# Kernel optimization log

Hardware: AMD Instinct MI355X
Metric: run time of the kernel (lower is better)

## Reference

```python
import jax, jax.numpy as jnp
import numpy as np

LN_EPS = 1e-5


def setup_inputs() -> dict:
    key = jax.random.key(0)
    k1, = jax.random.split(key, 1)
    B, C, H, W = 16, 512, 64, 64
    HW = H * W
    x = jax.random.normal(k1, (B, C, H, W), dtype=jnp.float32)
    gamma = jnp.ones((), dtype=jnp.float32)          # Scale(1) learnable scalar
    ln_weight = jnp.ones((HW,), dtype=jnp.float32)   # LayerNorm weight
    ln_bias = jnp.zeros((HW,), dtype=jnp.float32)    # LayerNorm bias
    return {"x": x, "gamma": gamma, "ln_weight": ln_weight, "ln_bias": ln_bias}


def reference(x, gamma, ln_weight, ln_bias):
    B, C, H, W = x.shape
    v = x.reshape(B, C, H * W)                       # [B, C, HW] (Q = K = V)
    energy = jnp.einsum('bcn,bdn->bcd', v, v)        # [B, C, C]
    attn = jax.nn.softmax(energy, axis=-1)
    out = jnp.einsum('bcd,bdn->bcn', attn, v)        # [B, C, HW]
    out = gamma * out + v                            # scale + residual
    # LayerNorm over last dim (HW), torch eps=1e-5
    mean = jnp.mean(out, axis=-1, keepdims=True)
    var = jnp.mean(jnp.square(out - mean), axis=-1, keepdims=True)
    out = (out - mean) * jax.lax.rsqrt(var + LN_EPS) * ln_weight + ln_bias
    return out.reshape(B, C, H, W)
```

## Files before the change

### kernel.cpp

```cpp
#include <hip/hip_runtime.h>
#include <hip/hip_bf16.h>

#define B_DIM 16
#define C_DIM 512
#define HW_DIM 4096
#define LN_EPS 1e-5f
#define ATTN_STRIDE 1024

using bf16 = __hip_bfloat16;
typedef __bf16 v8bf __attribute__((ext_vector_type(8)));
typedef float v4f __attribute__((ext_vector_type(4)));
typedef unsigned short v8us __attribute__((ext_vector_type(8)));
typedef unsigned short v4us __attribute__((ext_vector_type(4)));
using gptr_t = const __attribute__((address_space(1))) void*;
using lptr_t = __attribute__((address_space(3))) void*;

__device__ __forceinline__ unsigned short f2bf(float f) {
  unsigned int u = __float_as_uint(f);
  u = (u + 0x7fffu + ((u >> 16) & 1u)) >> 16;
  return (unsigned short)u;
}
__device__ __forceinline__ float bf2f(unsigned short us) {
  return __uint_as_float(((unsigned int)us) << 16);
}

__global__ __launch_bounds__(256) void k_convert(
    const float* __restrict__ x, unsigned short* __restrict__ v) {
  const size_t i0 = ((size_t)blockIdx.x * 256 + threadIdx.x) * 8;
  const size_t step = (size_t)2048 * 256 * 8;
#pragma unroll
  for (int it = 0; it < 8; ++it) {
    const size_t base = i0 + (size_t)it * step;
    const float4 f0 = ((const float4*)(x + base))[0];
    const float4 f1 = ((const float4*)(x + base))[1];
    v8us pack;
    pack[0] = f2bf(f0.x); pack[1] = f2bf(f0.y);
    pack[2] = f2bf(f0.z); pack[3] = f2bf(f0.w);
    pack[4] = f2bf(f1.x); pack[5] = f2bf(f1.y);
    pack[6] = f2bf(f1.z); pack[7] = f2bf(f1.w);
    *(v8us*)(v + base) = pack;
  }
}

#define TILE_E (256 * 64)

__device__ __forceinline__ void stage_half8(
    const bf16* __restrict__ g, bf16* l, int k0, int stride, int wave, int lane) {
  const int lrow = lane >> 3, lc = lane & 7;
#pragma unroll
  for (int i = 0; i < 2; ++i) {
    const int row = i * 64 + wave * 8 + lrow;
    __builtin_amdgcn_global_load_lds(
        (gptr_t)(g + (size_t)row * stride + k0 + ((lc ^ (row & 7)) << 3)),
        (lptr_t)(l + (i * 64 + wave * 8) * 64), 16, 0, 0);
  }
}
__device__ __forceinline__ void stage_op2(
    const bf16* __restrict__ g, bf16* l, int k0, int stride, int wave, int lane) {
  stage_half8(g, l, k0, stride, wave, lane);
  stage_half8(g + (size_t)128 * stride, l + 128 * 64, k0, stride, wave, lane);
}
__device__ __forceinline__ v8bf ld_frag8(const bf16* l, int row, int j) {
  return *(const v8bf*)(l + row * 64 + ((j ^ (row & 7)) << 3));
}
__device__ __forceinline__ v8bf ld_frag8B(const bf16* l, int row, int j) {
  const int key = (row & 7) ^ ((row >> 3) & 7);
  return *(const v8bf*)(l + row * 64 + ((j ^ key) << 3));
}
__device__ __forceinline__ void stageA8(
    const bf16* __restrict__ g, bf16* l, int k0, int stride,
    int w4, int lrow, int lc) {
#pragma unroll
  for (int i = 0; i < 8; ++i) {
    const int row = i * 32 + w4 * 8 + lrow;
    __builtin_amdgcn_global_load_lds(
        (gptr_t)(g + (size_t)row * stride + k0 + ((lc ^ (row & 7)) << 3)),
        (lptr_t)(l + (i * 32 + w4 * 8) * 64), 16, 0, 0);
  }
}
__device__ __forceinline__ void bwrite8(
    bf16* lb, const v8us bu[8], int dblk, int n8) {
  unsigned short* lu = (unsigned short*)lb;
#pragma unroll
  for (int j = 0; j < 8; ++j) {
    const int n = n8 + j;
    const int key = (n & 7) ^ ((n >> 3) & 7);
    v8us p;
#pragma unroll
    for (int r = 0; r < 8; ++r) p[r] = bu[r][j];
    *(v8us*)(lu + n * 64 + ((dblk ^ key) << 3)) = p;
  }
}

__device__ __forceinline__ void gemm_8ph_loop(
    const bf16* __restrict__ Ab, const bf16* __restrict__ Bb,
    const int strideA, const int strideB, const int kts,
    bf16* smem, const int wave, const int lane, v4f acc[8][4]) {
  const int wm = wave >> 2, wn = wave & 3;
  const int rl = lane & 15, kq = lane >> 4;

  stage_op2(Bb, smem + 2 * TILE_E, 0, strideB, wave, lane);
  stage_op2(Ab, smem, 0, strideA, wave, lane);
  stage_op2(Bb, smem + 3 * TILE_E, 64, strideB, wave, lane);
  stage_op2(Ab, smem + TILE_E, 64, strideA, wave, lane);
  asm volatile("s_waitcnt vmcnt(8)" ::: "memory");
  __builtin_amdgcn_s_barrier();

  v8bf a[4][2], b01[2][2], b23[2][2];
  for (int kt = 0; kt < kts; ++kt) {
    const bf16* LA = smem + (kt & 1) * TILE_E;
    const bf16* LB = smem + (2 + (kt & 1)) * TILE_E;
    bf16* SA = smem + (kt & 1) * TILE_E;
    bf16* SB = smem + (2 + (kt & 1)) * TILE_E;
#pragma unroll
    for (int mi = 0; mi < 4; ++mi)
#pragma unroll
      for (int kk = 0; kk < 2; ++kk)
        a[mi][kk] = ld_frag8(LA, wm * 128 + mi * 16 + rl, kk * 4 + kq);
#pragma unroll
    for (int ni = 0; ni < 2; ++ni)
#pragma unroll
      for (int kk = 0; kk < 2; ++kk)
        b01[ni][kk] = ld_frag8(LB, wn * 64 + ni * 16 + rl, kk * 4 + kq);
    __builtin_amdgcn_s_barrier();
    asm volatile("s_waitcnt lgkmcnt(0)");
    __builtin_amdgcn_s_setprio(1);
#pragma unroll
    for (int kk = 0; kk < 2; ++kk)
#pragma unroll
      for (int mi = 0; mi < 4; ++mi)
#pragma unroll
        for (int ni = 0; ni < 2; ++ni)
          acc[mi][ni] = __builtin_amdgcn_mfma_f32_16x16x32_bf16(
              a[mi][kk], b01[ni][kk], acc[mi][ni], 0, 0, 0);
    __builtin_amdgcn_s_setprio(0);
    __builtin_amdgcn_s_barrier();
#pragma unroll
    for (int ni = 0; ni < 2; ++ni)
#pragma unroll
      for (int kk = 0; kk < 2; ++kk)
        b23[ni][kk] = ld_frag8(LB, wn * 64 + (ni + 2) * 16 + rl, kk * 4 + kq);
    __builtin_amdgcn_s_barrier();
    asm volatile("s_waitcnt lgkmcnt(0)");
    __builtin_amdgcn_s_setprio(1);
#pragma unroll
    for (int kk = 0; kk < 2; ++kk)
#pragma unroll
      for (int mi = 0; mi < 4; ++mi)
#pragma unroll
        for (int ni = 0; ni < 2; ++ni)
          acc[mi][ni + 2] = __builtin_amdgcn_mfma_f32_16x16x32_bf16(
              a[mi][kk], b23[ni][kk], acc[mi][ni + 2], 0, 0, 0);
    __builtin_amdgcn_s_setprio(0);
    __builtin_amdgcn_s_barrier();
#pragma unroll
    for (int mi = 0; mi < 4; ++mi)
#pragma unroll
      for (int kk = 0; kk < 2; ++kk)
        a[mi][kk] = ld_frag8(LA, wm * 128 + (mi + 4) * 16 + rl, kk * 4 + kq);
    if (kt < kts - 2) stage_op2(Bb, SB, (kt + 2) * 64, strideB, wave, lane);
    __builtin_amdgcn_s_barrier();
    asm volatile("s_waitcnt lgkmcnt(0)");
    __builtin_amdgcn_s_setprio(1);
#pragma unroll
    for (int kk = 0; kk < 2; ++kk)
#pragma unroll
      for (int mi = 0; mi < 4; ++mi)
#pragma unroll
        for (int ni = 0; ni < 2; ++ni)
          acc[mi + 4][ni + 2] = __builtin_amdgcn_mfma_f32_16x16x32_bf16(
              a[mi][kk], b23[ni][kk], acc[mi + 4][ni + 2], 0, 0, 0);
    __builtin_amdgcn_s_setprio(0);
    __builtin_amdgcn_s_barrier();
    if (kt < kts - 2) stage_op2(Ab, SA, (kt + 2) * 64, strideA, wave, lane);
    __builtin_amdgcn_s_barrier();
    __builtin_amdgcn_s_setprio(1);
#pragma unroll
    for (int kk = 0; kk < 2; ++kk)
#pragma unroll
      for (int mi = 0; mi < 4; ++mi)
#pragma unroll
        for (int ni = 0; ni < 2; ++ni)
          acc[mi + 4][ni] = __builtin_amdgcn_mfma_f32_16x16x32_bf16(
              a[mi][kk], b01[ni][kk], acc[mi + 4][ni], 0, 0, 0);
    __builtin_amdgcn_s_setprio(0);
    if (kt < kts - 2)
      asm volatile("s_waitcnt vmcnt(8)" ::: "memory");
    else if (kt == kts - 2)
      asm volatile("s_waitcnt vmcnt(0)" ::: "memory");
    __builtin_amdgcn_s_barrier();
  }
}

__device__ __forceinline__ void epilogue_bounce(
    v4f acc[8][4], bf16* smem, float* ob, const int out_stride,
    const int wave, const int lane) {
  const int wm = wave >> 2, wn = wave & 3;
  const int rl = lane & 15, kq = lane >> 4;
  float* smf = (float*)smem;
#pragma unroll
  for (int h = 0; h < 2; ++h) {
    if (wm == h) {
#pragma unroll
      for (int mi = 0; mi < 8; ++mi)
#pragma unroll
        for (int ni = 0; ni < 4; ++ni)
#pragma unroll
          for (int rr = 0; rr < 4; ++rr) {
            const int rloc = mi * 16 + kq * 4 + rr;
            const int col = wn * 64 + ni * 16 + rl;
            const int key = rloc & 7;
            smf[rloc * 256 + ((((col >> 2) ^ key) << 2) | (col & 3))] =
                acc[mi][ni][rr];
          }
    }
    __syncthreads();
#pragma unroll
    for (int it = 0; it < 16; ++it) {
      const int rloc = it * 8 + wave;
      const float4 vv =
          *(const float4*)(smf + rloc * 256 + ((lane ^ (rloc & 7)) << 2));
      *(float4*)(ob + (size_t)(h * 128 + rloc) * out_stride + lane * 4) = vv;
    }
    __syncthreads();
  }
}

__global__ __launch_bounds__(512, 2) void k_gemm1(
    const bf16* __restrict__ v, float* __restrict__ e_part) {
  __shared__ __align__(16) bf16 smem[4 * TILE_E];
  const int bid = blockIdx.x;
  const int t = (bid & 7) * 32 + (bid >> 3);
  const int ks = t & 3;
  const int db = (t >> 2) & 1;
  const int cb = (t >> 3) & 1;
  const int b = t >> 4;
  const int tid = threadIdx.x;
  const int wave = tid >> 6, lane = tid & 63;

  const bf16* vb = v + (size_t)b * ((size_t)C_DIM * HW_DIM) + ks * 1024;
  const bf16* Ab = vb + (size_t)(cb * 256) * HW_DIM;
  const bf16* Bb = vb + (size_t)(db * 256) * HW_DIM;

  v4f acc[8][4] = {};
  gemm_8ph_loop(Ab, Bb, HW_DIM, HW_DIM, 16, smem, wave, lane, acc);

  float* ob = e_part + (size_t)ks * ((size_t)B_DIM * C_DIM * C_DIM) +
              (size_t)b * (C_DIM * C_DIM) + (size_t)(cb * 256) * C_DIM + db * 256;
  epilogue_bounce(acc, smem, ob, C_DIM, wave, lane);
}

__global__ __launch_bounds__(256) void k_softmax(
    const float* __restrict__ e_part, unsigned short* __restrict__ attn) {
  const int row = blockIdx.x;
  const size_t bcc = (size_t)B_DIM * C_DIM * C_DIM;
  const float* e0 = e_part + (size_t)row * C_DIM;
  const int tid = threadIdx.x;
  float v0 = 0.f, v1 = 0.f;
#pragma unroll
  for (int p = 0; p < 4; ++p) {
    v0 += e0[p * bcc + tid];
    v1 += e0[p * bcc + tid + 256];
  }
  float mx = fmaxf(v0, v1);
#pragma unroll
  for (int off = 32; off > 0; off >>= 1) mx = fmaxf(mx, __shfl_xor(mx, off));
  __shared__ float rmax[4], rsum[4];
  const int wv = tid >> 6, ln = tid & 63;
  if (ln == 0) rmax[wv] = mx;
  __syncthreads();
  mx = fmaxf(fmaxf(rmax[0], rmax[1]), fmaxf(rmax[2], rmax[3]));
  const float p0 = __expf(v0 - mx), p1 = __expf(v1 - mx);
  float s = p0 + p1;
#pragma unroll
  for (int off = 32; off > 0; off >>= 1) s += __shfl_xor(s, off);
  if (ln == 0) rsum[wv] = s;
  __syncthreads();
  s = rsum[0] + rsum[1] + rsum[2] + rsum[3];
  const float inv = 1.0f / s;
  attn[(size_t)row * ATTN_STRIDE + tid] = f2bf(p0 * inv);
  attn[(size_t)row * ATTN_STRIDE + tid + 256] = f2bf(p1 * inv);
}

__global__ __launch_bounds__(512, 2) void k_gemm2(
    const bf16* __restrict__ attn, const bf16* __restrict__ v,
    float* __restrict__ out) {
  __shared__ __align__(16) bf16 smem[4 * TILE_E];
  const int bid = blockIdx.x;
  const int t = (bid & 7) * 64 + (bid >> 3);
  const int b = t >> 5;
  const int cb = (t >> 4) & 1;
  const int nb = t & 15;
  const int tid = threadIdx.x;
  const int wave = tid >> 6, lane = tid & 63;
  const int rl = lane & 15, kq = lane >> 4;
  const int wm = wave >> 2, wn = wave & 3;

  const bf16* Ab = attn + (size_t)(b * C_DIM + cb * 256) * ATTN_STRIDE;
  const bf16* Vb = v + (size_t)b * ((size_t)C_DIM * HW_DIM) + nb * 256;

  const bool isB = (tid < 256);
  const int w4 = wave & 3;
  const int lrow = lane >> 3, lc = lane & 7;
  const int dblk = (tid & 255) >> 5;
  const int n8 = (tid & 31) * 8;

  v4f acc[8][4] = {};
  v8us bu[8];

  if (isB) {
#pragma unroll
    for (int r = 0; r < 8; ++r)
      bu[r] = *(const v8us*)((const unsigned short*)Vb +
                             (size_t)(dblk * 8 + r) * HW_DIM + n8);
    bwrite8(smem + 2 * TILE_E, bu, dblk, n8);
#pragma unroll
    for (int r = 0; r < 8; ++r)
      bu[r] = *(const v8us*)((const unsigned short*)Vb +
                             (size_t)(64 + dblk * 8 + r) * HW_DIM + n8);
    bwrite8(smem + 3 * TILE_E, bu, dblk, n8);
  } else {
    stageA8(Ab, smem, 0, ATTN_STRIDE, w4, lrow, lc);
    stageA8(Ab, smem + TILE_E, 64, ATTN_STRIDE, w4, lrow, lc);
  }
  asm volatile("s_waitcnt vmcnt(8)" ::: "memory");
  __builtin_amdgcn_s_barrier();

  v8bf a[4][2], b01[2][2], b23[2][2];
  for (int kt = 0; kt < 8; ++kt) {
    const bf16* LA = smem + (kt & 1) * TILE_E;
    const bf16* LB = smem + (2 + (kt & 1)) * TILE_E;
    bf16* SA = smem + (kt & 1) * TILE_E;
    bf16* SB = smem + (2 + (kt & 1)) * TILE_E;
#pragma unroll
    for (int mi = 0; mi < 4; ++mi)
#pragma unroll
      for (int kk = 0; kk < 2; ++kk)
        a[mi][kk] = ld_frag8(LA, wm * 128 + mi * 16 + rl, kk * 4 + kq);
#pragma unroll
    for (int ni = 0; ni < 2; ++ni)
#pragma unroll
      for (int kk = 0; kk < 2; ++kk)
        b01[ni][kk] = ld_frag8B(LB, wn * 64 + ni * 16 + rl, kk * 4 + kq);
    if (isB && kt < 6) {
      const int d0 = (kt + 2) * 64 + dblk * 8;
#pragma unroll
      for (int r = 0; r < 8; ++r)
        bu[r] = *(const v8us*)((const unsigned short*)Vb +
                               (size_t)(d0 + r) * HW_DIM + n8);
    }
    __builtin_amdgcn_s_barrier();
    asm volatile("s_waitcnt lgkmcnt(0)");
    __builtin_amdgcn_s_setprio(1);
#pragma unroll
    for (int kk = 0; kk < 2; ++kk)
#pragma unroll
      for (int mi = 0; mi < 4; ++mi)
#pragma unroll
        for (int ni = 0; ni < 2; ++ni)
          acc[mi][ni] = __builtin_amdgcn_mfma_f32_16x16x32_bf16(
              a[mi][kk], b01[ni][kk], acc[mi][ni], 0, 0, 0);
    __builtin_amdgcn_s_setprio(0);
    __builtin_amdgcn_s_barrier();
#pragma unroll
    for (int ni = 0; ni < 2; ++ni)
#pragma unroll
      for (int kk = 0; kk < 2; ++kk)
        b23[ni][kk] = ld_frag8B(LB, wn * 64 + (ni + 2) * 16 + rl, kk * 4 + kq);
    __builtin_amdgcn_s_barrier();
    asm volatile("s_waitcnt lgkmcnt(0)");
    __builtin_amdgcn_s_setprio(1);
#pragma unroll
    for (int kk = 0; kk < 2; ++kk)
#pragma unroll
      for (int mi = 0; mi < 4; ++mi)
#pragma unroll
        for (int ni = 0; ni < 2; ++ni)
          acc[mi][ni + 2] = __builtin_amdgcn_mfma_f32_16x16x32_bf16(
              a[mi][kk], b23[ni][kk], acc[mi][ni + 2], 0, 0, 0);
    __builtin_amdgcn_s_setprio(0);
    __builtin_amdgcn_s_barrier();
#pragma unroll
    for (int mi = 0; mi < 4; ++mi)
#pragma unroll
      for (int kk = 0; kk < 2; ++kk)
        a[mi][kk] = ld_frag8(LA, wm * 128 + (mi + 4) * 16 + rl, kk * 4 + kq);
    if (isB && kt < 6) bwrite8(SB, bu, dblk, n8);
    __builtin_amdgcn_s_barrier();
    asm volatile("s_waitcnt lgkmcnt(0)");
    __builtin_amdgcn_s_setprio(1);
#pragma unroll
    for (int kk = 0; kk < 2; ++kk)
#pragma unroll
      for (int mi = 0; mi < 4; ++mi)
#pragma unroll
        for (int ni = 0; ni < 2; ++ni)
          acc[mi + 4][ni + 2] = __builtin_amdgcn_mfma_f32_16x16x32_bf16(
              a[mi][kk], b23[ni][kk], acc[mi + 4][ni + 2], 0, 0, 0);
    __builtin_amdgcn_s_setprio(0);
    __builtin_amdgcn_s_barrier();
    if (!isB && kt < 6)
      stageA8(Ab, SA, (kt + 2) * 64, ATTN_STRIDE, w4, lrow, lc);
    __builtin_amdgcn_s_barrier();
    __builtin_amdgcn_s_setprio(1);
#pragma unroll
    for (int kk = 0; kk < 2; ++kk)
#pragma unroll
      for (int mi = 0; mi < 4; ++mi)
#pragma unroll
        for (int ni = 0; ni < 2; ++ni)
          acc[mi + 4][ni] = __builtin_amdgcn_mfma_f32_16x16x32_bf16(
              a[mi][kk], b01[ni][kk], acc[mi + 4][ni], 0, 0, 0);
    __builtin_amdgcn_s_setprio(0);
    if (kt < 6)
      asm volatile("s_waitcnt vmcnt(8)" ::: "memory");
    else if (kt == 6)
      asm volatile("s_waitcnt vmcnt(0)" ::: "memory");
    __builtin_amdgcn_s_barrier();
  }

  float* ob = out + (size_t)b * ((size_t)C_DIM * HW_DIM) +
              (size_t)(cb * 256) * HW_DIM + nb * 256;
  epilogue_bounce(acc, smem, ob, HW_DIM, wave, lane);
}

__global__ __launch_bounds__(256) void k_ln(
    float* __restrict__ out, const unsigned short* __restrict__ vres,
    const float* __restrict__ gamma, const float* __restrict__ w,
    const float* __restrict__ bias) {
  const int row = blockIdx.x;
  float* p = out + (size_t)row * HW_DIM;
  const unsigned short* vr = vres + (size_t)row * HW_DIM;
  const float g = gamma[0];
  const int tid = threadIdx.x;
  float4 vals[4];
  float s = 0.f, ss = 0.f;
#pragma unroll
  for (int i = 0; i < 4; ++i) {
    const int idx = tid + i * 256;
    const float4 av = ((const float4*)p)[idx];
    const v4us rv = *(const v4us*)(vr + idx * 4);
    float4 vv;
    vv.x = g * av.x + bf2f(rv[0]);
    vv.y = g * av.y + bf2f(rv[1]);
    vv.z = g * av.z + bf2f(rv[2]);
    vv.w = g * av.w + bf2f(rv[3]);
    vals[i] = vv;
    s += vv.x + vv.y + vv.z + vv.w;
    ss += vv.x * vv.x + vv.y * vv.y + vv.z * vv.z + vv.w * vv.w;
  }
#pragma unroll
  for (int off = 32; off > 0; off >>= 1) {
    s += __shfl_xor(s, off);
    ss += __shfl_xor(ss, off);
  }
  __shared__ float rs[4], rss[4];
  const int wv = tid >> 6, ln = tid & 63;
  if (ln == 0) { rs[wv] = s; rss[wv] = ss; }
  __syncthreads();
  s = rs[0] + rs[1] + rs[2] + rs[3];
  ss = rss[0] + rss[1] + rss[2] + rss[3];
  const float mean = s * (1.f / HW_DIM);
  const float var = ss * (1.f / HW_DIM) - mean * mean;
  const float rstd = rsqrtf(var + LN_EPS);
#pragma unroll
  for (int i = 0; i < 4; ++i) {
    const int idx = tid + i * 256;
    const float4 vv = vals[i];
    const float4 w4 = ((const float4*)w)[idx];
    const float4 b4 = ((const float4*)bias)[idx];
    float4 r;
    r.x = (vv.x - mean) * rstd * w4.x + b4.x;
    r.y = (vv.y - mean) * rstd * w4.y + b4.y;
    r.z = (vv.z - mean) * rstd * w4.z + b4.z;
    r.w = (vv.w - mean) * rstd * w4.w + b4.w;
    ((float4*)p)[idx] = r;
  }
}

extern "C" void kernel_launch(void* const* d_in, const int* in_sizes, int n_in,
                              void* d_out, int out_size, void* d_ws, size_t ws_size,
                              hipStream_t stream) {
  const float* x = (const float*)d_in[0];
  const float* gamma = (const float*)d_in[1];
  const float* lnw = (const float*)d_in[2];
  const float* lnb = (const float*)d_in[3];
  float* out = (float*)d_out;
  char* ws = (char*)d_ws;

  const size_t n_elem = (size_t)B_DIM * C_DIM * HW_DIM;
  unsigned short* vbf = (unsigned short*)ws;
  float* e_part = (float*)(ws + 4 * n_elem);
  unsigned short* attn = (unsigned short*)e_part;

  k_convert<<<2048, 256, 0, stream>>>(x, vbf);
  k_gemm1<<<256, 512, 0, stream>>>((const bf16*)vbf, e_part);
  k_softmax<<<B_DIM * C_DIM, 256, 0, stream>>>(e_part, attn);
  k_gemm2<<<512, 512, 0, stream>>>((const bf16*)attn, (const bf16*)vbf, out);
  k_ln<<<B_DIM * C_DIM, 256, 0, stream>>>(out, vbf, gamma, lnw, lnb);
}
```

Measured before the change: 243.4 us.

## Pre-transpose V during conversion, use async LDS loads in gemm2, emit bf16 intermediate

The conversion kernel now also writes a transposed bf16 copy of V ([n, c] layout) through a swizzled shared-memory tile. gemm2 can then stage both operands with global_load_lds, which replaces the register-based transpose and bwrite8 path. Attention rows are packed at stride C instead of 1024. gemm2 writes its output as bf16 into a workspace buffer rather than fp32 to the output, which halves that write and the matching read in the LayerNorm kernel. In exchange it adds an extra 64 MB transposed write and lowers the precision of the attention output before the residual and LayerNorm.

```diff
diff --git a/kernel.cpp b/kernel.cpp
--- a/kernel.cpp
+++ b/kernel.cpp
@@ -5,7 +5,6 @@
 #define C_DIM 512
 #define HW_DIM 4096
 #define LN_EPS 1e-5f
-#define ATTN_STRIDE 1024
 
 using bf16 = __hip_bfloat16;
 typedef __bf16 v8bf __attribute__((ext_vector_type(8)));
@@ -24,27 +23,58 @@
   return __uint_as_float(((unsigned int)us) << 16);
 }
 
-__global__ __launch_bounds__(256) void k_convert(
-    const float* __restrict__ x, unsigned short* __restrict__ v) {
-  const size_t i0 = ((size_t)blockIdx.x * 256 + threadIdx.x) * 8;
-  const size_t step = (size_t)2048 * 256 * 8;
-#pragma unroll
-  for (int it = 0; it < 8; ++it) {
-    const size_t base = i0 + (size_t)it * step;
-    const float4 f0 = ((const float4*)(x + base))[0];
-    const float4 f1 = ((const float4*)(x + base))[1];
+__global__ __launch_bounds__(256) void k_convert_transpose(
+    const float* __restrict__ x, unsigned short* __restrict__ v,
+    unsigned short* __restrict__ vt) {
+  __shared__ unsigned short tile[64 * 64];
+  const int tid = threadIdx.x;
+  const int b = blockIdx.z;
+  const int n0 = blockIdx.x * 64;
+  const int c0 = blockIdx.y * 64;
+  const size_t boff = (size_t)b * ((size_t)C_DIM * HW_DIM);
+  const float* xb = x + boff;
+  unsigned short* vb = v + boff;
+  unsigned short* vtb = vt + boff;
+
+  const int cl = tid >> 3;
+  const int hb = tid & 7;
+  const int h8 = hb * 8;
+#pragma unroll
+  for (int j = 0; j < 2; ++j) {
+    const int c = cl + j * 32;
+    const float* src = xb + (size_t)(c0 + c) * HW_DIM + n0 + h8;
+    const float4 f0 = ((const float4*)src)[0];
+    const float4 f1 = ((const float4*)src)[1];
     v8us pack;
     pack[0] = f2bf(f0.x); pack[1] = f2bf(f0.y);
     pack[2] = f2bf(f0.z); pack[3] = f2bf(f0.w);
     pack[4] = f2bf(f1.x); pack[5] = f2bf(f1.y);
     pack[6] = f2bf(f1.z); pack[7] = f2bf(f1.w);
-    *(v8us*)(v + base) = pack;
-  }
+    *(v8us*)(vb + (size_t)(c0 + c) * HW_DIM + n0 + h8) = pack;
+    const int key = (c & 7) ^ ((c >> 3) & 7);
+    *(v8us*)(tile + c * 64 + ((hb ^ key) << 3)) = pack;
+  }
+  __syncthreads();
+  const int nl = tid >> 3;
+  const int c8 = (tid & 7) * 8;
+  const int n = 2 * nl;
+  v8us pa, pb;
+#pragma unroll
+  for (int e = 0; e < 8; ++e) {
+    const int r = c8 + e;
+    const int key = (r & 7) ^ ((r >> 3) & 7);
+    const unsigned int w = *(const unsigned int*)(
+        tile + r * 64 + (((n >> 3) ^ key) << 3) + (n & 7));
+    pa[e] = (unsigned short)(w & 0xffffu);
+    pb[e] = (unsigned short)(w >> 16);
+  }
+  *(v8us*)(vtb + (size_t)(n0 + n) * C_DIM + c0 + c8) = pa;
+  *(v8us*)(vtb + (size_t)(n0 + n + 1) * C_DIM + c0 + c8) = pb;
 }
 
 #define TILE_E (256 * 64)
 
-__device__ __forceinline__ void stage_half8(
+__device__ __forceinline__ void stage_half8s(
     const bf16* __restrict__ g, bf16* l, int k0, int stride, int wave, int lane) {
   const int lrow = lane >> 3, lc = lane & 7;
 #pragma unroll
@@ -55,41 +85,29 @@
         (lptr_t)(l + (i * 64 + wave * 8) * 64), 16, 0, 0);
   }
 }
+__device__ __forceinline__ void stage_op2s(
+    const bf16* __restrict__ g, bf16* l, int k0, int stride, int wave, int lane) {
+  stage_half8s(g, l, k0, stride, wave, lane);
+  stage_half8s(g + (size_t)128 * stride, l + 128 * 64, k0, stride, wave, lane);
+}
+__device__ __forceinline__ void stage_half8(
+    const bf16* __restrict__ g, bf16* l, int k0, int wave, int lane) {
+  const int lrow = lane >> 3, lc = lane & 7;
+#pragma unroll
+  for (int i = 0; i < 2; ++i) {
+    const int row = i * 64 + wave * 8 + lrow;
+    __builtin_amdgcn_global_load_lds(
+        (gptr_t)(g + (size_t)row * C_DIM + k0 + ((lc ^ (row & 7)) << 3)),
+        (lptr_t)(l + (i * 64 + wave * 8) * 64), 16, 0, 0);
+  }
+}
 __device__ __forceinline__ void stage_op2(
-    const bf16* __restrict__ g, bf16* l, int k0, int stride, int wave, int lane) {
-  stage_half8(g, l, k0, stride, wave, lane);
-  stage_half8(g + (size_t)128 * stride, l + 128 * 64, k0, stride, wave, lane);
+    const bf16* __restrict__ g, bf16* l, int k0, int wave, int lane) {
+  stage_half8(g, l, k0, wave, lane);
+  stage_half8(g + (size_t)128 * C_DIM, l + 128 * 64, k0, wave, lane);
 }
 __device__ __forceinline__ v8bf ld_frag8(const bf16* l, int row, int j) {
   return *(const v8bf*)(l + row * 64 + ((j ^ (row & 7)) << 3));
-}
-__device__ __forceinline__ v8bf ld_frag8B(const bf16* l, int row, int j) {
-  const int key = (row & 7) ^ ((row >> 3) & 7);
-  return *(const v8bf*)(l + row * 64 + ((j ^ key) << 3));
-}
-__device__ __forceinline__ void stageA8(
-    const bf16* __restrict__ g, bf16* l, int k0, int stride,
-    int w4, int lrow, int lc) {
-#pragma unroll
-  for (int i = 0; i < 8; ++i) {
-    const int row = i * 32 + w4 * 8 + lrow;
-    __builtin_amdgcn_global_load_lds(
-        (gptr_t)(g + (size_t)row * stride + k0 + ((lc ^ (row & 7)) << 3)),
-        (lptr_t)(l + (i * 32 + w4 * 8) * 64), 16, 0, 0);
-  }
-}
-__device__ __forceinline__ void bwrite8(
-    bf16* lb, const v8us bu[8], int dblk, int n8) {
-  unsigned short* lu = (unsigned short*)lb;
-#pragma unroll
-  for (int j = 0; j < 8; ++j) {
-    const int n = n8 + j;
-    const int key = (n & 7) ^ ((n >> 3) & 7);
-    v8us p;
-#pragma unroll
-    for (int r = 0; r < 8; ++r) p[r] = bu[r][j];
-    *(v8us*)(lu + n * 64 + ((dblk ^ key) << 3)) = p;
-  }
 }
 
 __device__ __forceinline__ void gemm_8ph_loop(
@@ -99,10 +117,10 @@
   const int wm = wave >> 2, wn = wave & 3;
   const int rl = lane & 15, kq = lane >> 4;
 
-  stage_op2(Bb, smem + 2 * TILE_E, 0, strideB, wave, lane);
-  stage_op2(Ab, smem, 0, strideA, wave, lane);
-  stage_op2(Bb, smem + 3 * TILE_E, 64, strideB, wave, lane);
-  stage_op2(Ab, smem + TILE_E, 64, strideA, wave, lane);
+  stage_op2s(Bb, smem + 2 * TILE_E, 0, strideB, wave, lane);
+  stage_op2s(Ab, smem, 0, strideA, wave, lane);
+  stage_op2s(Bb, smem + 3 * TILE_E, 64, strideB, wave, lane);
+  stage_op2s(Ab, smem + TILE_E, 64, strideA, wave, lane);
   asm volatile("s_waitcnt vmcnt(8)" ::: "memory");
   __builtin_amdgcn_s_barrier();
 
@@ -158,7 +176,7 @@
 #pragma unroll
       for (int kk = 0; kk < 2; ++kk)
         a[mi][kk] = ld_frag8(LA, wm * 128 + (mi + 4) * 16 + rl, kk * 4 + kq);
-    if (kt < kts - 2) stage_op2(Bb, SB, (kt + 2) * 64, strideB, wave, lane);
+    if (kt < kts - 2) stage_op2s(Bb, SB, (kt + 2) * 64, strideB, wave, lane);
     __builtin_amdgcn_s_barrier();
     asm volatile("s_waitcnt lgkmcnt(0)");
     __builtin_amdgcn_s_setprio(1);
@@ -172,7 +190,7 @@
               a[mi][kk], b23[ni][kk], acc[mi + 4][ni + 2], 0, 0, 0);
     __builtin_amdgcn_s_setprio(0);
     __builtin_amdgcn_s_barrier();
-    if (kt < kts - 2) stage_op2(Ab, SA, (kt + 2) * 64, strideA, wave, lane);
+    if (kt < kts - 2) stage_op2s(Ab, SA, (kt + 2) * 64, strideA, wave, lane);
     __builtin_amdgcn_s_barrier();
     __builtin_amdgcn_s_setprio(1);
 #pragma unroll
@@ -278,13 +296,13 @@
   __syncthreads();
   s = rsum[0] + rsum[1] + rsum[2] + rsum[3];
   const float inv = 1.0f / s;
-  attn[(size_t)row * ATTN_STRIDE + tid] = f2bf(p0 * inv);
-  attn[(size_t)row * ATTN_STRIDE + tid + 256] = f2bf(p1 * inv);
+  attn[(size_t)row * C_DIM + tid] = f2bf(p0 * inv);
+  attn[(size_t)row * C_DIM + tid + 256] = f2bf(p1 * inv);
 }
 
 __global__ __launch_bounds__(512, 2) void k_gemm2(
-    const bf16* __restrict__ attn, const bf16* __restrict__ v,
-    float* __restrict__ out) {
+    const bf16* __restrict__ attn, const bf16* __restrict__ vt,
+    unsigned short* __restrict__ av) {
   __shared__ __align__(16) bf16 smem[4 * TILE_E];
   const int bid = blockIdx.x;
   const int t = (bid & 7) * 64 + (bid >> 3);
@@ -293,36 +311,18 @@
   const int nb = t & 15;
   const int tid = threadIdx.x;
   const int wave = tid >> 6, lane = tid & 63;
+  const int wm = wave >> 2, wn = wave & 3;
   const int rl = lane & 15, kq = lane >> 4;
-  const int wm = wave >> 2, wn = wave & 3;
-
-  const bf16* Ab = attn + (size_t)(b * C_DIM + cb * 256) * ATTN_STRIDE;
-  const bf16* Vb = v + (size_t)b * ((size_t)C_DIM * HW_DIM) + nb * 256;
-
-  const bool isB = (tid < 256);
-  const int w4 = wave & 3;
-  const int lrow = lane >> 3, lc = lane & 7;
-  const int dblk = (tid & 255) >> 5;
-  const int n8 = (tid & 31) * 8;
+
+  const bf16* Ab = attn + (size_t)b * (C_DIM * C_DIM) + (size_t)(cb * 256) * C_DIM;
+  const bf16* Bb = vt + (size_t)b * ((size_t)C_DIM * HW_DIM) + (size_t)(nb * 256) * C_DIM;
 
   v4f acc[8][4] = {};
-  v8us bu[8];
-
-  if (isB) {
-#pragma unroll
-    for (int r = 0; r < 8; ++r)
-      bu[r] = *(const v8us*)((const unsigned short*)Vb +
-                             (size_t)(dblk * 8 + r) * HW_DIM + n8);
-    bwrite8(smem + 2 * TILE_E, bu, dblk, n8);
-#pragma unroll
-    for (int r = 0; r < 8; ++r)
-      bu[r] = *(const v8us*)((const unsigned short*)Vb +
-                             (size_t)(64 + dblk * 8 + r) * HW_DIM + n8);
-    bwrite8(smem + 3 * TILE_E, bu, dblk, n8);
-  } else {
-    stageA8(Ab, smem, 0, ATTN_STRIDE, w4, lrow, lc);
-    stageA8(Ab, smem + TILE_E, 64, ATTN_STRIDE, w4, lrow, lc);
-  }
+
+  stage_op2(Bb, smem + 2 * TILE_E, 0, wave, lane);
+  stage_op2(Ab, smem, 0, wave, lane);
+  stage_op2(Bb, smem + 3 * TILE_E, 64, wave, lane);
+  stage_op2(Ab, smem + TILE_E, 64, wave, lane);
   asm volatile("s_waitcnt vmcnt(8)" ::: "memory");
   __builtin_amdgcn_s_barrier();
 
@@ -341,14 +341,7 @@
     for (int ni = 0; ni < 2; ++ni)
 #pragma unroll
       for (int kk = 0; kk < 2; ++kk)
-        b01[ni][kk] = ld_frag8B(LB, wn * 64 + ni * 16 + rl, kk * 4 + kq);
-    if (isB && kt < 6) {
-      const int d0 = (kt + 2) * 64 + dblk * 8;
-#pragma unroll
-      for (int r = 0; r < 8; ++r)
-        bu[r] = *(const v8us*)((const unsigned short*)Vb +
-                               (size_t)(d0 + r) * HW_DIM + n8);
-    }
+        b01[ni][kk] = ld_frag8(LB, wn * 64 + ni * 16 + rl, kk * 4 + kq);
     __builtin_amdgcn_s_barrier();
     asm volatile("s_waitcnt lgkmcnt(0)");
     __builtin_amdgcn_s_setprio(1);
@@ -366,7 +359,7 @@
     for (int ni = 0; ni < 2; ++ni)
 #pragma unroll
       for (int kk = 0; kk < 2; ++kk)
-        b23[ni][kk] = ld_frag8B(LB, wn * 64 + (ni + 2) * 16 + rl, kk * 4 + kq);
+        b23[ni][kk] = ld_frag8(LB, wn * 64 + (ni + 2) * 16 + rl, kk * 4 + kq);
     __builtin_amdgcn_s_barrier();
     asm volatile("s_waitcnt lgkmcnt(0)");
     __builtin_amdgcn_s_setprio(1);
@@ -385,7 +378,7 @@
 #pragma unroll
       for (int kk = 0; kk < 2; ++kk)
         a[mi][kk] = ld_frag8(LA, wm * 128 + (mi + 4) * 16 + rl, kk * 4 + kq);
-    if (isB && kt < 6) bwrite8(SB, bu, dblk, n8);
+    if (kt < 6) stage_op2(Bb, SB, (kt + 2) * 64, wave, lane);
     __builtin_amdgcn_s_barrier();
     asm volatile("s_waitcnt lgkmcnt(0)");
     __builtin_amdgcn_s_setprio(1);
@@ -399,8 +392,7 @@
               a[mi][kk], b23[ni][kk], acc[mi + 4][ni + 2], 0, 0, 0);
     __builtin_amdgcn_s_setprio(0);
     __builtin_amdgcn_s_barrier();
-    if (!isB && kt < 6)
-      stageA8(Ab, SA, (kt + 2) * 64, ATTN_STRIDE, w4, lrow, lc);
+    if (kt < 6) stage_op2(Ab, SA, (kt + 2) * 64, wave, lane);
     __builtin_amdgcn_s_barrier();
     __builtin_amdgcn_s_setprio(1);
 #pragma unroll
@@ -419,17 +411,48 @@
     __builtin_amdgcn_s_barrier();
   }
 
-  float* ob = out + (size_t)b * ((size_t)C_DIM * HW_DIM) +
-              (size_t)(cb * 256) * HW_DIM + nb * 256;
-  epilogue_bounce(acc, smem, ob, HW_DIM, wave, lane);
+  float* smf = (float*)smem;
+  unsigned short* ob = av + (size_t)b * ((size_t)C_DIM * HW_DIM) +
+                       (size_t)(cb * 256) * HW_DIM + nb * 256;
+#pragma unroll
+  for (int h = 0; h < 2; ++h) {
+    if (wm == h) {
+#pragma unroll
+      for (int mi = 0; mi < 8; ++mi)
+#pragma unroll
+        for (int ni = 0; ni < 4; ++ni)
+#pragma unroll
+          for (int rr = 0; rr < 4; ++rr) {
+            const int rloc = mi * 16 + kq * 4 + rr;
+            const int col = wn * 64 + ni * 16 + rl;
+            const int key = rloc & 7;
+            smf[rloc * 256 + ((((col >> 2) ^ key) << 2) | (col & 3))] =
+                acc[mi][ni][rr];
+          }
+    }
+    __syncthreads();
+#pragma unroll
+    for (int it = 0; it < 16; ++it) {
+      const int rloc = it * 8 + wave;
+      const float4 vv =
+          *(const float4*)(smf + rloc * 256 + ((lane ^ (rloc & 7)) << 2));
+      v4us p;
+      p[0] = f2bf(vv.x); p[1] = f2bf(vv.y);
+      p[2] = f2bf(vv.z); p[3] = f2bf(vv.w);
+      *(v4us*)(ob + (size_t)(h * 128 + rloc) * HW_DIM + lane * 4) = p;
+    }
+    __syncthreads();
+  }
 }
 
 __global__ __launch_bounds__(256) void k_ln(
-    float* __restrict__ out, const unsigned short* __restrict__ vres,
+    float* __restrict__ out, const unsigned short* __restrict__ av,
+    const unsigned short* __restrict__ vres,
     const float* __restrict__ gamma, const float* __restrict__ w,
     const float* __restrict__ bias) {
   const int row = blockIdx.x;
   float* p = out + (size_t)row * HW_DIM;
+  const unsigned short* ap = av + (size_t)row * HW_DIM;
   const unsigned short* vr = vres + (size_t)row * HW_DIM;
   const float g = gamma[0];
   const int tid = threadIdx.x;
@@ -438,13 +461,13 @@
 #pragma unroll
   for (int i = 0; i < 4; ++i) {
     const int idx = tid + i * 256;
-    const float4 av = ((const float4*)p)[idx];
+    const v4us au = *(const v4us*)(ap + idx * 4);
     const v4us rv = *(const v4us*)(vr + idx * 4);
     float4 vv;
-    vv.x = g * av.x + bf2f(rv[0]);
-    vv.y = g * av.y + bf2f(rv[1]);
-    vv.z = g * av.z + bf2f(rv[2]);
-    vv.w = g * av.w + bf2f(rv[3]);
+    vv.x = g * bf2f(au[0]) + bf2f(rv[0]);
+    vv.y = g * bf2f(au[1]) + bf2f(rv[1]);
+    vv.z = g * bf2f(au[2]) + bf2f(rv[2]);
+    vv.w = g * bf2f(au[3]) + bf2f(rv[3]);
     vals[i] = vv;
     s += vv.x + vv.y + vv.z + vv.w;
     ss += vv.x * vv.x + vv.y * vv.y + vv.z * vv.z + vv.w * vv.w;
@@ -489,13 +512,20 @@
   char* ws = (char*)d_ws;
 
   const size_t n_elem = (size_t)B_DIM * C_DIM * HW_DIM;
+  const size_t e_elems = (size_t)B_DIM * C_DIM * C_DIM;
   unsigned short* vbf = (unsigned short*)ws;
+  unsigned short* vbfT = (unsigned short*)(ws + 2 * n_elem);
   float* e_part = (float*)(ws + 4 * n_elem);
-  unsigned short* attn = (unsigned short*)e_part;
-
-  k_convert<<<2048, 256, 0, stream>>>(x, vbf);
+  unsigned short* attn =
+      (unsigned short*)(ws + 4 * n_elem + 4 * e_elems * sizeof(float));
+  unsigned short* av = (unsigned short*)(ws + 4 * n_elem +
+                                         4 * e_elems * sizeof(float) +
+                                         2 * e_elems);
+
+  k_convert_transpose<<<dim3(HW_DIM / 64, C_DIM / 64, B_DIM), 256, 0, stream>>>(
+      x, vbf, vbfT);
   k_gemm1<<<256, 512, 0, stream>>>((const bf16*)vbf, e_part);
   k_softmax<<<B_DIM * C_DIM, 256, 0, stream>>>(e_part, attn);
-  k_gemm2<<<512, 512, 0, stream>>>((const bf16*)attn, (const bf16*)vbf, out);
-  k_ln<<<B_DIM * C_DIM, 256, 0, stream>>>(out, vbf, gamma, lnw, lnb);
-}
+  k_gemm2<<<512, 512, 0, stream>>>((const bf16*)attn, (const bf16*)vbfT, av);
+  k_ln<<<B_DIM * C_DIM, 256, 0, stream>>>(out, av, vbf, gamma, lnw, lnb);
+}
```

After: 212.9 us, median of 2. 12.5% less time.
